# Optimization experiments

Measured on AMD Instinct MI355X. Metric: run time of the kernel, lower is better.

Reference implementation:

```python
import jax, jax.numpy as jnp
import numpy as np

B, H, S, D = 2, 16, 2048, 64
SCALE = 1.0 / float(np.sqrt(D))


def setup_inputs() -> dict:
    key = jax.random.key(0)
    kq, kk, kv = jax.random.split(key, 3)
    q = jax.random.normal(kq, (B, H, S, D), dtype=jnp.float32)
    k = jax.random.normal(kk, (B, H, S, D), dtype=jnp.float32)
    v = jax.random.normal(kv, (B, H, S, D), dtype=jnp.float32)
    return {"q": q, "k": k, "v": v}


def reference(q, k, v):
    # scores: [B, H, Sq, Sk] -- module materializes full attention weights
    scores = jnp.einsum("bhqd,bhkd->bhqk", q * SCALE, k)
    attn_weights = jax.nn.softmax(scores, axis=-1)
    out = jnp.einsum("bhqk,bhkd->bhqd", attn_weights, v)
    return (out, attn_weights)
```

## Files before the change

kernel.cpp:

```cpp
#include <hip/hip_runtime.h>
#include <hip/hip_bf16.h>

namespace {

constexpr int Bc = 2, Hc = 16, Sc = 2048, Dc = 64;
constexpr float kScale = 0.125f;
constexpr int KC = 64;
constexpr int NT = Sc / KC;

typedef __attribute__((ext_vector_type(8))) short bf16x8;
typedef __attribute__((ext_vector_type(4))) short s16x4;
typedef __attribute__((ext_vector_type(4))) float f32x4;

__device__ inline short f2bf(float x) {
    union { float f; unsigned int u; } v;
    v.f = x;
    unsigned int r = v.u + 0x7fffu + ((v.u >> 16) & 1u);
    return (short)(r >> 16);
}

__device__ inline void gload16(const void* g, void* l) {
    typedef __attribute__((address_space(1))) const unsigned int GU;
    typedef __attribute__((address_space(3))) unsigned int LU;
    __builtin_amdgcn_global_load_lds((GU*)g, (LU*)l, 16, 0, 0);
}

__global__ __launch_bounds__(256)
void prep(const float* __restrict__ kg, const float* __restrict__ vg,
          unsigned short* __restrict__ kb, unsigned short* __restrict__ vtb) {
    const int tid = (int)threadIdx.x;
    const int bh = (int)blockIdx.y;
    const int k0 = (int)blockIdx.x * KC;
    const float* kh = kg + (size_t)bh * Sc * Dc;
    const float* vh = vg + (size_t)bh * Sc * Dc;
    unsigned short* kbh = kb + (size_t)bh * Sc * Dc;
    unsigned short* vth = vtb + (size_t)bh * Sc * Dc;

    __shared__ float sv[64][65];

    #pragma unroll
    for (int it = 0; it < 4; ++it) {
        int fid = tid + it * 256;
        int row = fid >> 4;
        int c4  = (fid & 15) * 4;
        int key = k0 + row;
        float4 tk = *(const float4*)(kh + (size_t)key * Dc + c4);
        int dsw = c4 ^ ((key & 7) << 3);
        s16x4 kv;
        kv[0] = f2bf(tk.x); kv[1] = f2bf(tk.y); kv[2] = f2bf(tk.z); kv[3] = f2bf(tk.w);
        *(s16x4*)(kbh + (size_t)key * Dc + dsw) = kv;
        float4 tv = *(const float4*)(vh + (size_t)key * Dc + c4);
        sv[row][c4 + 0] = tv.x; sv[row][c4 + 1] = tv.y;
        sv[row][c4 + 2] = tv.z; sv[row][c4 + 3] = tv.w;
    }
    __syncthreads();

    const int d = tid >> 2;
    const int key16 = (tid & 3) * 16;
    const int s = (d & 7) << 3;
    const int base = key16 ^ (s & 48);
    const int b0 = base + (s & 8);
    const int b1 = base + ((s & 8) ^ 8);
    bf16x8 r0, r1;
    #pragma unroll
    for (int i = 0; i < 8; ++i) {
        r0[i] = f2bf(sv[key16 + i][d]);
        r1[i] = f2bf(sv[key16 + 8 + i][d]);
    }
    *(bf16x8*)(vth + (size_t)d * Sc + k0 + b0) = r0;
    *(bf16x8*)(vth + (size_t)d * Sc + k0 + b1) = r1;
}

__device__ inline void stage_k_tile(const unsigned short* kbh, int k0,
                                    unsigned short* dst, int tid) {
    const unsigned short* src = kbh + (size_t)k0 * Dc;
    gload16(src + tid * 8, dst + tid * 8);
    gload16(src + 2048 + tid * 8, dst + 2048 + tid * 8);
}
__device__ inline void stage_vt_tile(const unsigned short* vth, int k0,
                                     unsigned short* dst, int tid) {
    int r = tid >> 3, c8 = (tid & 7) * 8;
    gload16(vth + (size_t)r * Sc + k0 + c8, dst + r * 64 + c8);
    gload16(vth + (size_t)(r + 32) * Sc + k0 + c8, dst + (r + 32) * 64 + c8);
}

__global__ __launch_bounds__(256, 4)
void fa_fwd(const float* __restrict__ qg, const unsigned short* __restrict__ kb,
            const unsigned short* __restrict__ vtb, float* __restrict__ outg,
            float* __restrict__ attng) {
    const int tid  = (int)threadIdx.x;
    const int wave = tid >> 6;
    const int lane = tid & 63;
    const int m16  = lane & 15;
    const int q4   = lane >> 4;
    const int sw   = (m16 & 7) << 3;

    const int bh = (int)blockIdx.y;
    const int qw = (int)blockIdx.x * 64 + wave * 16;

    __shared__ __align__(16) unsigned short s_k[2][64][64];
    __shared__ __align__(16) unsigned short s_vt[2][64][64];
    __shared__ __align__(16) unsigned short s_p[4][16][64];

    const float* qh = qg + (size_t)bh * Sc * Dc;
    const unsigned short* kbh = kb + (size_t)bh * Sc * Dc;
    const unsigned short* vth = vtb + (size_t)bh * Sc * Dc;
    float* oh = outg + (size_t)bh * Sc * Dc;
    float* ph = attng + (size_t)bh * Sc * Sc;

    bf16x8 a0, a1;
    {
        const float* qr = qh + (size_t)(qw + m16) * Dc + q4 * 8;
        #pragma unroll
        for (int j = 0; j < 8; ++j) {
            a0[j] = f2bf(qr[j] * kScale);
            a1[j] = f2bf(qr[j + 32] * kScale);
        }
    }

    float m_i = -1e30f, l_i = 0.0f;

    stage_k_tile(kbh, 0, &s_k[0][0][0], tid);
    __syncthreads();
    for (int t = 0; t < NT; ++t) {
        const int cur = t & 1;
        if (t + 1 < NT) stage_k_tile(kbh, (t + 1) * KC, &s_k[cur ^ 1][0][0], tid);

        float sc[4][4];
        #pragma unroll
        for (int kt = 0; kt < 4; ++kt) {
            const unsigned short* kp = &s_k[cur][kt * 16 + m16][0];
            bf16x8 b0 = *(const bf16x8*)(kp + ((q4 * 8) ^ sw));
            bf16x8 b1 = *(const bf16x8*)(kp + ((q4 * 8 + 32) ^ sw));
            f32x4 c = {0.f, 0.f, 0.f, 0.f};
            c = __builtin_amdgcn_mfma_f32_16x16x32_bf16(b0, a0, c, 0, 0, 0);
            c = __builtin_amdgcn_mfma_f32_16x16x32_bf16(b1, a1, c, 0, 0, 0);
            #pragma unroll
            for (int r = 0; r < 4; ++r) sc[kt][r] = c[r];
        }

        float tmax = sc[0][0];
        #pragma unroll
        for (int kt = 0; kt < 4; ++kt)
            #pragma unroll
            for (int r = 0; r < 4; ++r) tmax = fmaxf(tmax, sc[kt][r]);
        tmax = fmaxf(tmax, __shfl_xor(tmax, 16));
        tmax = fmaxf(tmax, __shfl_xor(tmax, 32));

        const float mn = fmaxf(m_i, tmax);
        float tsum = 0.f;
        #pragma unroll
        for (int kt = 0; kt < 4; ++kt)
            #pragma unroll
            for (int r = 0; r < 4; ++r) tsum += __expf(sc[kt][r] - mn);
        tsum += __shfl_xor(tsum, 16);
        tsum += __shfl_xor(tsum, 32);

        l_i = l_i * __expf(m_i - mn) + tsum;
        m_i = mn;
        __syncthreads();
    }
    const float inv_l = 1.0f / l_i;

    f32x4 o[4];
    #pragma unroll
    for (int dt = 0; dt < 4; ++dt) o[dt] = (f32x4){0.f, 0.f, 0.f, 0.f};

    stage_k_tile(kbh, 0, &s_k[0][0][0], tid);
    stage_vt_tile(vth, 0, &s_vt[0][0][0], tid);
    __syncthreads();
    for (int t = 0; t < NT; ++t) {
        const int cur = t & 1;
        const int k0 = t * KC;
        if (t + 1 < NT) {
            stage_k_tile(kbh, k0 + KC, &s_k[cur ^ 1][0][0], tid);
            stage_vt_tile(vth, k0 + KC, &s_vt[cur ^ 1][0][0], tid);
        }

        #pragma unroll
        for (int kt = 0; kt < 4; ++kt) {
            const unsigned short* kp = &s_k[cur][kt * 16 + m16][0];
            bf16x8 b0 = *(const bf16x8*)(kp + ((q4 * 8) ^ sw));
            bf16x8 b1 = *(const bf16x8*)(kp + ((q4 * 8 + 32) ^ sw));
            f32x4 c = {0.f, 0.f, 0.f, 0.f};
            c = __builtin_amdgcn_mfma_f32_16x16x32_bf16(b0, a0, c, 0, 0, 0);
            c = __builtin_amdgcn_mfma_f32_16x16x32_bf16(b1, a1, c, 0, 0, 0);
            float4 p4;
            p4.x = __expf(c[0] - m_i) * inv_l;
            p4.y = __expf(c[1] - m_i) * inv_l;
            p4.z = __expf(c[2] - m_i) * inv_l;
            p4.w = __expf(c[3] - m_i) * inv_l;
            *(float4*)(ph + (size_t)(qw + m16) * Sc + k0 + kt * 16 + q4 * 4) = p4;
            s16x4 pk;
            pk[0] = f2bf(p4.x); pk[1] = f2bf(p4.y);
            pk[2] = f2bf(p4.z); pk[3] = f2bf(p4.w);
            *(s16x4*)(&s_p[wave][m16][(kt * 16 + q4 * 4) ^ sw]) = pk;
        }

        #pragma unroll
        for (int kh2 = 0; kh2 < 2; ++kh2) {
            bf16x8 pa = *(const bf16x8*)(&s_p[wave][m16][(kh2 * 32 + q4 * 8) ^ sw]);
            #pragma unroll
            for (int dt = 0; dt < 4; ++dt) {
                bf16x8 vb = *(const bf16x8*)(&s_vt[cur][dt * 16 + m16][(kh2 * 32 + q4 * 8) ^ sw]);
                o[dt] = __builtin_amdgcn_mfma_f32_16x16x32_bf16(pa, vb, o[dt], 0, 0, 0);
            }
        }
        __syncthreads();
    }

    #pragma unroll
    for (int dt = 0; dt < 4; ++dt)
        #pragma unroll
        for (int r = 0; r < 4; ++r)
            oh[(size_t)(qw + q4 * 4 + r) * Dc + dt * 16 + m16] = o[dt][r];
}

}

extern "C" void kernel_launch(void* const* d_in, const int* in_sizes, int n_in,
                              void* d_out, int out_size, void* d_ws, size_t ws_size,
                              hipStream_t stream) {
    (void)in_sizes; (void)n_in; (void)out_size; (void)ws_size;
    const float* q = (const float*)d_in[0];
    const float* k = (const float*)d_in[1];
    const float* v = (const float*)d_in[2];
    float* out  = (float*)d_out;
    float* attn = out + (size_t)Bc * Hc * Sc * Dc;

    const size_t n = (size_t)Bc * Hc * Sc * Dc;
    unsigned short* kb  = (unsigned short*)d_ws;
    unsigned short* vtb = kb + n;

    dim3 grid(Sc / KC, Bc * Hc);
    prep<<<grid, 256, 0, stream>>>(k, v, kb, vtb);
    fa_fwd<<<grid, 256, 0, stream>>>(q, kb, vtb, out, attn);
}
```

Measured before the change: 689.6 us.

## Pre-swizzle K/V into MFMA fragment order and load directly from global

The prep kernel now writes K and V^T in per-lane MFMA fragment order, so the attention kernel reads operands straight from global or L2 with contiguous 16-byte loads. This removes LDS staging and the per-tile block barriers. It also folds log2(e) into the Q scale so the softmax can use exp2f, switches the attention-weight stores to nontemporal, and remaps the 1D grid so blocks that share a head run close together for L2 reuse. In exchange, every wave re-reads K and V from cache without LDS sharing, which may raise L2 traffic.

```diff
diff --git a/kernel.cpp b/kernel.cpp
--- a/kernel.cpp
+++ b/kernel.cpp
@@ -1,12 +1,11 @@
 #include <hip/hip_runtime.h>
-#include <hip/hip_bf16.h>
 
 namespace {
 
 constexpr int Bc = 2, Hc = 16, Sc = 2048, Dc = 64;
-constexpr float kScale = 0.125f;
 constexpr int KC = 64;
 constexpr int NT = Sc / KC;
+constexpr float kQScale = 0.125f * 1.4426950408889634f;
 
 typedef __attribute__((ext_vector_type(8))) short bf16x8;
 typedef __attribute__((ext_vector_type(4))) short s16x4;
@@ -19,74 +18,60 @@
     return (short)(r >> 16);
 }
 
-__device__ inline void gload16(const void* g, void* l) {
-    typedef __attribute__((address_space(1))) const unsigned int GU;
-    typedef __attribute__((address_space(3))) unsigned int LU;
-    __builtin_amdgcn_global_load_lds((GU*)g, (LU*)l, 16, 0, 0);
-}
-
 __global__ __launch_bounds__(256)
 void prep(const float* __restrict__ kg, const float* __restrict__ vg,
-          unsigned short* __restrict__ kb, unsigned short* __restrict__ vtb) {
+          unsigned short* __restrict__ kf, unsigned short* __restrict__ vf) {
     const int tid = (int)threadIdx.x;
     const int bh = (int)blockIdx.y;
     const int k0 = (int)blockIdx.x * KC;
     const float* kh = kg + (size_t)bh * Sc * Dc;
     const float* vh = vg + (size_t)bh * Sc * Dc;
-    unsigned short* kbh = kb + (size_t)bh * Sc * Dc;
-    unsigned short* vth = vtb + (size_t)bh * Sc * Dc;
+    unsigned short* kfh = kf + (size_t)bh * Sc * Dc;
+    unsigned short* vfh = vf + (size_t)bh * Sc * Dc;
 
     __shared__ float sv[64][65];
 
     #pragma unroll
     for (int it = 0; it < 4; ++it) {
         int fid = tid + it * 256;
-        int row = fid >> 4;
-        int c4  = (fid & 15) * 4;
-        int key = k0 + row;
-        float4 tk = *(const float4*)(kh + (size_t)key * Dc + c4);
-        int dsw = c4 ^ ((key & 7) << 3);
-        s16x4 kv;
-        kv[0] = f2bf(tk.x); kv[1] = f2bf(tk.y); kv[2] = f2bf(tk.z); kv[3] = f2bf(tk.w);
-        *(s16x4*)(kbh + (size_t)key * Dc + dsw) = kv;
-        float4 tv = *(const float4*)(vh + (size_t)key * Dc + c4);
+        int row = fid >> 4, c4 = (fid & 15) * 4;
+        float4 tv = *(const float4*)(vh + (size_t)(k0 + row) * Dc + c4);
         sv[row][c4 + 0] = tv.x; sv[row][c4 + 1] = tv.y;
         sv[row][c4 + 2] = tv.z; sv[row][c4 + 3] = tv.w;
     }
+
+    #pragma unroll
+    for (int it = 0; it < 2; ++it) {
+        int idx = tid + it * 256;
+        int r = idx >> 3, g8 = idx & 7;
+        int row = k0 + r;
+        const float* kr = kh + (size_t)row * Dc + g8 * 8;
+        float4 t0 = *(const float4*)kr;
+        float4 t1 = *(const float4*)(kr + 4);
+        bf16x8 kv;
+        kv[0] = f2bf(t0.x); kv[1] = f2bf(t0.y); kv[2] = f2bf(t0.z); kv[3] = f2bf(t0.w);
+        kv[4] = f2bf(t1.x); kv[5] = f2bf(t1.y); kv[6] = f2bf(t1.z); kv[7] = f2bf(t1.w);
+        int di = (((row >> 4) * 2 + (g8 >> 2)) * 64 + (row & 15) + ((g8 & 3) << 4)) * 8;
+        *(bf16x8*)(kfh + di) = kv;
+    }
     __syncthreads();
 
-    const int d = tid >> 2;
-    const int key16 = (tid & 3) * 16;
-    const int s = (d & 7) << 3;
-    const int base = key16 ^ (s & 48);
-    const int b0 = base + (s & 8);
-    const int b1 = base + ((s & 8) ^ 8);
-    bf16x8 r0, r1;
-    #pragma unroll
-    for (int i = 0; i < 8; ++i) {
-        r0[i] = f2bf(sv[key16 + i][d]);
-        r1[i] = f2bf(sv[key16 + 8 + i][d]);
-    }
-    *(bf16x8*)(vth + (size_t)d * Sc + k0 + b0) = r0;
-    *(bf16x8*)(vth + (size_t)d * Sc + k0 + b1) = r1;
-}
-
-__device__ inline void stage_k_tile(const unsigned short* kbh, int k0,
-                                    unsigned short* dst, int tid) {
-    const unsigned short* src = kbh + (size_t)k0 * Dc;
-    gload16(src + tid * 8, dst + tid * 8);
-    gload16(src + 2048 + tid * 8, dst + 2048 + tid * 8);
-}
-__device__ inline void stage_vt_tile(const unsigned short* vth, int k0,
-                                     unsigned short* dst, int tid) {
-    int r = tid >> 3, c8 = (tid & 7) * 8;
-    gload16(vth + (size_t)r * Sc + k0 + c8, dst + r * 64 + c8);
-    gload16(vth + (size_t)(r + 32) * Sc + k0 + c8, dst + (r + 32) * 64 + c8);
+    #pragma unroll
+    for (int it = 0; it < 2; ++it) {
+        int idx = tid + it * 256;
+        int d = idx >> 3, o = idx & 7;
+        int g = (k0 >> 5) + (o >> 2);
+        bf16x8 vv;
+        #pragma unroll
+        for (int i = 0; i < 8; ++i) vv[i] = f2bf(sv[o * 8 + i][d]);
+        int di = ((g * 4 + (d >> 4)) * 64 + (d & 15) + ((o & 3) << 4)) * 8;
+        *(bf16x8*)(vfh + di) = vv;
+    }
 }
 
 __global__ __launch_bounds__(256, 4)
-void fa_fwd(const float* __restrict__ qg, const unsigned short* __restrict__ kb,
-            const unsigned short* __restrict__ vtb, float* __restrict__ outg,
+void fa_fwd(const float* __restrict__ qg, const unsigned short* __restrict__ kf,
+            const unsigned short* __restrict__ vf, float* __restrict__ outg,
             float* __restrict__ attng) {
     const int tid  = (int)threadIdx.x;
     const int wave = tid >> 6;
@@ -95,16 +80,16 @@
     const int q4   = lane >> 4;
     const int sw   = (m16 & 7) << 3;
 
-    const int bh = (int)blockIdx.y;
-    const int qw = (int)blockIdx.x * 64 + wave * 16;
-
-    __shared__ __align__(16) unsigned short s_k[2][64][64];
-    __shared__ __align__(16) unsigned short s_vt[2][64][64];
+    const int flat = (int)blockIdx.x;
+    const int bh   = (((flat >> 8) & 3) << 3) | (flat & 7);
+    const int qb   = (flat >> 3) & 31;
+    const int qw   = qb * 64 + wave * 16;
+
     __shared__ __align__(16) unsigned short s_p[4][16][64];
 
     const float* qh = qg + (size_t)bh * Sc * Dc;
-    const unsigned short* kbh = kb + (size_t)bh * Sc * Dc;
-    const unsigned short* vth = vtb + (size_t)bh * Sc * Dc;
+    const unsigned short* kfh = kf + (size_t)bh * Sc * Dc;
+    const unsigned short* vfh = vf + (size_t)bh * Sc * Dc;
     float* oh = outg + (size_t)bh * Sc * Dc;
     float* ph = attng + (size_t)bh * Sc * Sc;
 
@@ -113,32 +98,28 @@
         const float* qr = qh + (size_t)(qw + m16) * Dc + q4 * 8;
         #pragma unroll
         for (int j = 0; j < 8; ++j) {
-            a0[j] = f2bf(qr[j] * kScale);
-            a1[j] = f2bf(qr[j + 32] * kScale);
-        }
-    }
+            a0[j] = f2bf(qr[j] * kQScale);
+            a1[j] = f2bf(qr[j + 32] * kQScale);
+        }
+    }
+
+    const unsigned short* kl = kfh + lane * 8;
+    const unsigned short* vl = vfh + lane * 8;
 
     float m_i = -1e30f, l_i = 0.0f;
-
-    stage_k_tile(kbh, 0, &s_k[0][0][0], tid);
-    __syncthreads();
     for (int t = 0; t < NT; ++t) {
-        const int cur = t & 1;
-        if (t + 1 < NT) stage_k_tile(kbh, (t + 1) * KC, &s_k[cur ^ 1][0][0], tid);
-
+        const unsigned short* kt_base = kl + t * 4096;
         float sc[4][4];
         #pragma unroll
         for (int kt = 0; kt < 4; ++kt) {
-            const unsigned short* kp = &s_k[cur][kt * 16 + m16][0];
-            bf16x8 b0 = *(const bf16x8*)(kp + ((q4 * 8) ^ sw));
-            bf16x8 b1 = *(const bf16x8*)(kp + ((q4 * 8 + 32) ^ sw));
+            bf16x8 b0 = *(const bf16x8*)(kt_base + kt * 1024);
+            bf16x8 b1 = *(const bf16x8*)(kt_base + kt * 1024 + 512);
             f32x4 c = {0.f, 0.f, 0.f, 0.f};
             c = __builtin_amdgcn_mfma_f32_16x16x32_bf16(b0, a0, c, 0, 0, 0);
             c = __builtin_amdgcn_mfma_f32_16x16x32_bf16(b1, a1, c, 0, 0, 0);
             #pragma unroll
             for (int r = 0; r < 4; ++r) sc[kt][r] = c[r];
         }
-
         float tmax = sc[0][0];
         #pragma unroll
         for (int kt = 0; kt < 4; ++kt)
@@ -152,13 +133,12 @@
         #pragma unroll
         for (int kt = 0; kt < 4; ++kt)
             #pragma unroll
-            for (int r = 0; r < 4; ++r) tsum += __expf(sc[kt][r] - mn);
+            for (int r = 0; r < 4; ++r) tsum += exp2f(sc[kt][r] - mn);
         tsum += __shfl_xor(tsum, 16);
         tsum += __shfl_xor(tsum, 32);
 
-        l_i = l_i * __expf(m_i - mn) + tsum;
+        l_i = l_i * exp2f(m_i - mn) + tsum;
         m_i = mn;
-        __syncthreads();
     }
     const float inv_l = 1.0f / l_i;
 
@@ -166,34 +146,25 @@
     #pragma unroll
     for (int dt = 0; dt < 4; ++dt) o[dt] = (f32x4){0.f, 0.f, 0.f, 0.f};
 
-    stage_k_tile(kbh, 0, &s_k[0][0][0], tid);
-    stage_vt_tile(vth, 0, &s_vt[0][0][0], tid);
-    __syncthreads();
     for (int t = 0; t < NT; ++t) {
-        const int cur = t & 1;
-        const int k0 = t * KC;
-        if (t + 1 < NT) {
-            stage_k_tile(kbh, k0 + KC, &s_k[cur ^ 1][0][0], tid);
-            stage_vt_tile(vth, k0 + KC, &s_vt[cur ^ 1][0][0], tid);
-        }
+        const unsigned short* kt_base = kl + t * 4096;
+        const unsigned short* vt_base = vl + t * 4096;
 
         #pragma unroll
         for (int kt = 0; kt < 4; ++kt) {
-            const unsigned short* kp = &s_k[cur][kt * 16 + m16][0];
-            bf16x8 b0 = *(const bf16x8*)(kp + ((q4 * 8) ^ sw));
-            bf16x8 b1 = *(const bf16x8*)(kp + ((q4 * 8 + 32) ^ sw));
+            bf16x8 b0 = *(const bf16x8*)(kt_base + kt * 1024);
+            bf16x8 b1 = *(const bf16x8*)(kt_base + kt * 1024 + 512);
             f32x4 c = {0.f, 0.f, 0.f, 0.f};
             c = __builtin_amdgcn_mfma_f32_16x16x32_bf16(b0, a0, c, 0, 0, 0);
             c = __builtin_amdgcn_mfma_f32_16x16x32_bf16(b1, a1, c, 0, 0, 0);
-            float4 p4;
-            p4.x = __expf(c[0] - m_i) * inv_l;
-            p4.y = __expf(c[1] - m_i) * inv_l;
-            p4.z = __expf(c[2] - m_i) * inv_l;
-            p4.w = __expf(c[3] - m_i) * inv_l;
-            *(float4*)(ph + (size_t)(qw + m16) * Sc + k0 + kt * 16 + q4 * 4) = p4;
+            f32x4 p4;
+            #pragma unroll
+            for (int r = 0; r < 4; ++r) p4[r] = exp2f(c[r] - m_i) * inv_l;
+            __builtin_nontemporal_store(
+                p4, (f32x4*)(ph + (size_t)(qw + m16) * Sc + t * 64 + kt * 16 + q4 * 4));
             s16x4 pk;
-            pk[0] = f2bf(p4.x); pk[1] = f2bf(p4.y);
-            pk[2] = f2bf(p4.z); pk[3] = f2bf(p4.w);
+            pk[0] = f2bf(p4[0]); pk[1] = f2bf(p4[1]);
+            pk[2] = f2bf(p4[2]); pk[3] = f2bf(p4[3]);
             *(s16x4*)(&s_p[wave][m16][(kt * 16 + q4 * 4) ^ sw]) = pk;
         }
 
@@ -202,11 +173,10 @@
             bf16x8 pa = *(const bf16x8*)(&s_p[wave][m16][(kh2 * 32 + q4 * 8) ^ sw]);
             #pragma unroll
             for (int dt = 0; dt < 4; ++dt) {
-                bf16x8 vb = *(const bf16x8*)(&s_vt[cur][dt * 16 + m16][(kh2 * 32 + q4 * 8) ^ sw]);
+                bf16x8 vb = *(const bf16x8*)(vt_base + kh2 * 2048 + dt * 512);
                 o[dt] = __builtin_amdgcn_mfma_f32_16x16x32_bf16(pa, vb, o[dt], 0, 0, 0);
             }
         }
-        __syncthreads();
     }
 
     #pragma unroll
@@ -229,10 +199,9 @@
     float* attn = out + (size_t)Bc * Hc * Sc * Dc;
 
     const size_t n = (size_t)Bc * Hc * Sc * Dc;
-    unsigned short* kb  = (unsigned short*)d_ws;
-    unsigned short* vtb = kb + n;
-
-    dim3 grid(Sc / KC, Bc * Hc);
-    prep<<<grid, 256, 0, stream>>>(k, v, kb, vtb);
-    fa_fwd<<<grid, 256, 0, stream>>>(q, kb, vtb, out, attn);
-}
+    unsigned short* kf = (unsigned short*)d_ws;
+    unsigned short* vf = kf + n;
+
+    prep<<<dim3(Sc / KC, Bc * Hc), 256, 0, stream>>>(k, v, kf, vf);
+    fa_fwd<<<dim3((Sc / 64) * Bc * Hc), 256, 0, stream>>>(q, kf, vf, out, attn);
+}
```

Measured after the change: 647.1 us. -6.2%, faster.
